# Optimization experiments

Measured on AMD Instinct MI355X. Metric: run time of the kernel, lower is better.

## Reference

```python
import jax, jax.numpy as jnp
import numpy as np
from itertools import product

L0 = (41, 1600, 1408)  # sparse_shape (z,y,x) from pc_range / voxel_size + [1,0,0]
B = 4
N_PER = 25000
PNAMES = ['w_in','s_in','b_in','w1','s1','b1','w2a','s2a','b2a','w2b','s2b','b2b','w2c','s2c','b2c','w3a','s3a','b3a','w3b','s3b','b3b','w3c','s3c','b3c','w4a','s4a','b4a','w4b','s4b','b4b','w4c','s4c','b4c','w_out','s_out','b_out']


def _enc(c, shape):
    D, H, W = shape
    return ((c[:, 0].astype(np.int64) * D + c[:, 1]) * H + c[:, 2]) * W + c[:, 3]


def _subm_rb(coords, shape):
    # submanifold conv rulebook: out site i gathers input j with coord_j = coord_i + offset
    N = coords.shape[0]
    keys = _enc(coords, shape)
    order = np.argsort(keys); sk = keys[order]
    ins, outs = [], []
    for dz, dy, dx in product((-1, 0, 1), repeat=3):
        nb = coords.astype(np.int64).copy()
        nb[:, 1] += dz; nb[:, 2] += dy; nb[:, 3] += dx
        ok = ((nb[:, 1] >= 0) & (nb[:, 1] < shape[0]) & (nb[:, 2] >= 0) & (nb[:, 2] < shape[1]) & (nb[:, 3] >= 0) & (nb[:, 3] < shape[2]))
        qi = np.nonzero(ok)[0]
        qk = _enc(nb[qi], shape)
        pos = np.clip(np.searchsorted(sk, qk), 0, N - 1)
        f = sk[pos] == qk
        ins.append(order[pos[f]].astype(np.int32))
        outs.append(qi[f].astype(np.int32))
    R = max(len(a) for a in ins)
    rin = np.zeros((27, R), np.int32); rout = np.full((27, R), N, np.int32)  # pad -> dummy out row
    for k in range(27):
        rin[k, :len(ins[k])] = ins[k]; rout[k, :len(outs[k])] = outs[k]
    return jnp.asarray(rin), jnp.asarray(rout)


def _spconv_rb(coords, shape, ks, st, pd):
    # strided sparse conv: out = (in + pad - k) / stride where divisible and in-bounds
    osh = tuple((shape[i] + 2 * pd[i] - ks[i]) // st[i] + 1 for i in range(3))
    per = []; allk = []
    for off in product(*[range(k) for k in ks]):
        oc = np.empty((coords.shape[0], 4), np.int64)
        oc[:, 0] = coords[:, 0]
        ok = np.ones(coords.shape[0], bool)
        for d in range(3):
            v = coords[:, d + 1].astype(np.int64) + pd[d] - off[d]
            ok &= (v % st[d] == 0)
            v = v // st[d]
            ok &= (v >= 0) & (v < osh[d])
            oc[:, d + 1] = v
        qi = np.nonzero(ok)[0]
        qk = _enc(oc[qi], osh)
        per.append((qi.astype(np.int32), qk)); allk.append(qk)
    uk = np.unique(np.concatenate(allk))
    Nout = len(uk); K = len(per)
    R = max(len(qi) for qi, _ in per)
    rin = np.zeros((K, R), np.int32); rout = np.full((K, R), Nout, np.int32)
    for k, (qi, qk) in enumerate(per):
        rin[k, :len(qi)] = qi
        rout[k, :len(qi)] = np.searchsorted(uk, qk).astype(np.int32)
    t = uk.copy()
    x = t % osh[2]; t //= osh[2]; y = t % osh[1]; t //= osh[1]; z = t % osh[0]; b = t // osh[0]
    ocoords = np.stack([b, z, y, x], 1).astype(np.int32)
    return jnp.asarray(rin), jnp.asarray(rout), ocoords, osh


def _gen_coords(rng):
    # clustered LiDAR-like voxel occupancy: gaussian clusters so 3x3x3 neighborhoods are populated
    out = []
    for b in range(B):
        nc = 250
        ctr = np.stack([rng.integers(6, 34, nc), rng.integers(60, 1540, nc), rng.integers(60, 1348, nc)], 1)
        pts = ctr[np.repeat(np.arange(nc), 400)] + rng.normal(0.0, 2.0, (nc * 400, 3))
        pts = np.rint(pts).astype(np.int64)
        for d in range(3):
            pts[:, d] = np.clip(pts[:, d], 0, L0[d] - 1)
        keys = (pts[:, 0] * L0[1] + pts[:, 1]) * L0[2] + pts[:, 2]
        _, ui = np.unique(keys, return_index=True)
        assert len(ui) >= N_PER
        c = pts[np.sort(ui[:N_PER])]
        out.append(np.concatenate([np.full((N_PER, 1), b, np.int64), c], 1))
    return np.concatenate(out, 0).astype(np.int32)


def _conv(feat, W, rin, rout, nout):
    # gather -> per-offset GEMM -> scatter-add (spconv rulebook algorithm)
    out = jnp.zeros((nout + 1, W.shape[2]), feat.dtype)  # +1 dummy row for padding
    for k in range(W.shape[0]):
        out = out.at[rout[k]].add(feat[rin[k]] @ W[k])
    return out[:nout]


def _bnrelu(x, s, b):
    # eval-mode BatchNorm1d folded to affine, then ReLU
    return jax.nn.relu(x * s + b)


def _net(voxels, normalizer, rb1_in, rb1_out, rb2s_in, rb2s_out, batch2, rb2_in, rb2_out, rb3s_in, rb3s_out, batch3, rb3_in, rb3_out, rb4s_in, rb4s_out, batch4, rb4_in, rb4_out, rbo_in, rbo_out, batch_out, P):
    n0 = voxels.shape[0]; n2 = batch2.shape[0]; n3 = batch3.shape[0]; n4 = batch4.shape[0]; no = batch_out.shape[0]
    f = voxels.sum(1) / normalizer  # mean VFE: (N0, 4)
    x = _bnrelu(_conv(f, P['w_in'], rb1_in, rb1_out, n0), P['s_in'], P['b_in'])
    x = _bnrelu(_conv(x, P['w1'], rb1_in, rb1_out, n0), P['s1'], P['b1'])
    x = _bnrelu(_conv(x, P['w2a'], rb2s_in, rb2s_out, n2), P['s2a'], P['b2a'])
    x = _bnrelu(_conv(x, P['w2b'], rb2_in, rb2_out, n2), P['s2b'], P['b2b'])
    x = _bnrelu(_conv(x, P['w2c'], rb2_in, rb2_out, n2), P['s2c'], P['b2c'])
    x = _bnrelu(_conv(x, P['w3a'], rb3s_in, rb3s_out, n3), P['s3a'], P['b3a'])
    x = _bnrelu(_conv(x, P['w3b'], rb3_in, rb3_out, n3), P['s3b'], P['b3b'])
    x = _bnrelu(_conv(x, P['w3c'], rb3_in, rb3_out, n3), P['s3c'], P['b3c'])
    x = _bnrelu(_conv(x, P['w4a'], rb4s_in, rb4s_out, n4), P['s4a'], P['b4a'])
    x = _bnrelu(_conv(x, P['w4b'], rb4_in, rb4_out, n4), P['s4b'], P['b4b'])
    x = _bnrelu(_conv(x, P['w4c'], rb4_in, rb4_out, n4), P['s4c'], P['b4c'])
    x = _bnrelu(_conv(x, P['w_out'], rbo_in, rbo_out, no), P['s_out'], P['b_out'])
    # per-batch global max pool over active voxels (== F.max_pool1d over voxel dim)
    return jax.ops.segment_max(x, batch_out.astype(jnp.int32), num_segments=B)


def setup_inputs():
    rng = np.random.default_rng(0)
    coords0 = _gen_coords(rng)
    rb1_in, rb1_out = _subm_rb(coords0, L0)
    rb2s_in, rb2s_out, c2, sh2 = _spconv_rb(coords0, L0, (3, 3, 3), (2, 2, 2), (1, 1, 1))
    rb2_in, rb2_out = _subm_rb(c2, sh2)
    rb3s_in, rb3s_out, c3, sh3 = _spconv_rb(c2, sh2, (3, 3, 3), (2, 2, 2), (1, 1, 1))
    rb3_in, rb3_out = _subm_rb(c3, sh3)
    rb4s_in, rb4s_out, c4, sh4 = _spconv_rb(c3, sh3, (3, 3, 3), (2, 2, 2), (0, 1, 1))
    rb4_in, rb4_out = _subm_rb(c4, sh4)
    rbo_in, rbo_out, co, _ = _spconv_rb(c4, sh4, (3, 1, 1), (2, 1, 1), (0, 0, 0))
    N0 = coords0.shape[0]
    d = dict(
        voxels=jnp.asarray(rng.normal(0, 1, (N0, 5, 4)).astype(np.float32)),
        voxel_num_points=jnp.asarray(rng.integers(1, 6, N0).astype(np.int32)),
        voxel_coords=jnp.asarray(coords0),
        rb1_in=rb1_in, rb1_out=rb1_out,
        rb2s_in=rb2s_in, rb2s_out=rb2s_out, batch2=jnp.asarray(c2[:, 0]),
        rb2_in=rb2_in, rb2_out=rb2_out,
        rb3s_in=rb3s_in, rb3s_out=rb3s_out, batch3=jnp.asarray(c3[:, 0]),
        rb3_in=rb3_in, rb3_out=rb3_out,
        rb4s_in=rb4s_in, rb4s_out=rb4s_out, batch4=jnp.asarray(c4[:, 0]),
        rb4_in=rb4_in, rb4_out=rb4_out,
        rbo_in=rbo_in, rbo_out=rbo_out, batch_out=jnp.asarray(co[:, 0]),
    )
    def _w(k, ci, co_):
        return jnp.asarray((rng.normal(0, 1, (k, ci, co_)) / np.sqrt(k * ci)).astype(np.float32))
    def _bn(c):
        return (jnp.asarray(rng.uniform(0.5, 1.5, c).astype(np.float32)), jnp.asarray(rng.normal(0, 0.1, c).astype(np.float32)))
    d['w_in'] = _w(27, 4, 16); d['s_in'], d['b_in'] = _bn(16)
    d['w1'] = _w(27, 16, 16); d['s1'], d['b1'] = _bn(16)
    d['w2a'] = _w(27, 16, 32); d['s2a'], d['b2a'] = _bn(32)
    d['w2b'] = _w(27, 32, 32); d['s2b'], d['b2b'] = _bn(32)
    d['w2c'] = _w(27, 32, 32); d['s2c'], d['b2c'] = _bn(32)
    d['w3a'] = _w(27, 32, 64); d['s3a'], d['b3a'] = _bn(64)
    d['w3b'] = _w(27, 64, 64); d['s3b'], d['b3b'] = _bn(64)
    d['w3c'] = _w(27, 64, 64); d['s3c'], d['b3c'] = _bn(64)
    d['w4a'] = _w(27, 64, 64); d['s4a'], d['b4a'] = _bn(64)
    d['w4b'] = _w(27, 64, 64); d['s4b'], d['b4b'] = _bn(64)
    d['w4c'] = _w(27, 64, 64); d['s4c'], d['b4c'] = _bn(64)
    d['w_out'] = _w(3, 64, 128); d['s_out'], d['b_out'] = _bn(128)
    return d


def reference(voxels, voxel_num_points, voxel_coords, rb1_in, rb1_out, rb2s_in, rb2s_out, batch2, rb2_in, rb2_out, rb3s_in, rb3s_out, batch3, rb3_in, rb3_out, rb4s_in, rb4s_out, batch4, rb4_in, rb4_out, rbo_in, rbo_out, batch_out, w_in, s_in, b_in, w1, s1, b1, w2a, s2a, b2a, w2b, s2b, b2b, w2c, s2c, b2c, w3a, s3a, b3a, w3b, s3b, b3b, w3c, s3c, b3c, w4a, s4a, b4a, w4b, s4b, b4b, w4c, s4c, b4c, w_out, s_out, b_out):
    normalizer = jnp.maximum(voxel_num_points.astype(voxels.dtype), 1.0)[:, None]
    P = dict(zip(PNAMES, (w_in, s_in, b_in, w1, s1, b1, w2a, s2a, b2a, w2b, s2b, b2b, w2c, s2c, b2c, w3a, s3a, b3a, w3b, s3b, b3b, w3c, s3c, b3c, w4a, s4a, b4a, w4b, s4b, b4b, w4c, s4c, b4c, w_out, s_out, b_out)))
    return _net(voxels, normalizer, rb1_in, rb1_out, rb2s_in, rb2s_out, batch2, rb2_in, rb2_out, rb3s_in, rb3s_out, batch3, rb3_in, rb3_out, rb4s_in, rb4s_out, batch4, rb4_in, rb4_out, rbo_in, rbo_out, batch_out, P)
```

## Files before the change

kernel.cpp:

```cpp
#include <hip/hip_runtime.h>
#include <cstddef>
#include <cstdint>

typedef _Float16 half8 __attribute__((ext_vector_type(8)));
typedef float floatx4 __attribute__((ext_vector_type(4)));
typedef float floatx16 __attribute__((ext_vector_type(16)));

static inline int cdiv_i(int a, int b) { return (a + b - 1) / b; }

struct RB { const int* rin; const int* rout; int K, R, nout, start, end, off; };
struct RBs { RB d[8]; };
__global__ void rb_fill_all(RBs P, int* __restrict__ tbl, int total) {
  int idx = blockIdx.x * blockDim.x + threadIdx.x;
  if (idx >= total) return;
#pragma unroll
  for (int l = 0; l < 8; ++l) {
    if (idx >= P.d[l].start && idx < P.d[l].end) {
      const RB rb = P.d[l];
      int e = idx - rb.start;
      int o = rb.rout[e];
      if ((unsigned)o < (unsigned)rb.nout) {
        int k = e / rb.R;
        tbl[rb.off + (size_t)k * rb.nout + o] = rb.rin[e];
      }
    }
  }
}

__global__ void tbl_fill_kernel(const int* __restrict__ rin,
                                const int* __restrict__ rout,
                                int* __restrict__ tbl, int K, int R, int nout) {
  int e = blockIdx.x * blockDim.x + threadIdx.x;
  if (e >= K * R) return;
  int o = rout[e];
  if ((unsigned)o >= (unsigned)nout) return;
  int k = e / R;
  tbl[(size_t)k * nout + o] = rin[e];
}

struct WP { const float* W; int K, Ci, CiPad, Co, start, end, off, p32; };
struct WPs {
  WP d[12];
  const float* vox; const int* vnp; _Float16* f0; int featTot, N0;
  float* dout; int outTot;
  int* tbl; int tblTot;
};
__global__ void prep_all(WPs P, _Float16* __restrict__ Bp, int total) {
  int idx = blockIdx.x * blockDim.x + threadIdx.x;
  if (idx >= total) return;
  if (idx < P.featTot) {
    int i = idx >> 3, c = idx & 7;
    float v = 0.f;
    if (i < P.N0 && c < 4) {
      const float* p = P.vox + (size_t)i * 20 + c;
      v = (p[0] + p[4] + p[8] + p[12] + p[16]) / fmaxf((float)P.vnp[i], 1.f);
    }
    P.f0[idx] = (_Float16)v;
    return;
  }
  idx -= P.featTot;
  if (idx < P.outTot) {
    P.dout[idx] = 0.f;
    return;
  }
  idx -= P.outTot;
  if (idx < P.tblTot) {
    P.tbl[idx] = -1;
    return;
  }
  int widx = idx - P.tblTot;
#pragma unroll
  for (int l = 0; l < 12; ++l) {
    if (widx >= P.d[l].start && widx < P.d[l].end) {
      const WP w = P.d[l];
      int e = widx - w.start;
      int j = e & 7;
      int lane = (e >> 3) & 63;
      int rest = e >> 9;
      float v;
      if (w.p32) {
        int NT = w.Co >> 5;
        int t = rest % NT, ch = rest / NT;
        int SUB = w.CiPad >> 4;
        int ko = ch / SUB, s = ch % SUB;
        int ci = s * 16 + ((lane >> 5) << 3) + j;
        int col = t * 32 + (lane & 31);
        v = w.W[((size_t)ko * w.Ci + ci) * w.Co + col];
      } else {
        int NT = w.Co >> 4;
        int t = rest % NT, ch = rest / NT;
        int kk = ch * 32 + ((lane >> 4) << 3) + j;
        int k = kk / w.CiPad, ci = kk % w.CiPad;
        int n = t * 16 + (lane & 15);
        v = (k < w.K && ci < w.Ci) ? w.W[((size_t)k * w.Ci + ci) * w.Co + n] : 0.f;
      }
      Bp[w.off + e] = (_Float16)v;
    }
  }
}

template <int K, int CiPad, int Co, int KS, int CG, int CBLK>
__global__ __launch_bounds__(256) void conv_mfma(
    const _Float16* __restrict__ feat, const _Float16* __restrict__ Bp,
    const int* __restrict__ tbl, const float* __restrict__ sc,
    const float* __restrict__ bi, _Float16* __restrict__ out,
    int nout, int nin) {
  constexpr int NT = Co / 16;
  constexpr int NTE = NT / CBLK;
  constexpr int NTW = NTE / CG;
  constexpr int RG = 4 / (KS * CG);
  static_assert(KS * CG * RG == 4 && RG >= 1 && NT % CBLK == 0 && NTE % CG == 0);
  constexpr int NCH = (K * CiPad + 31) / 32;
  constexpr int L2C = (CiPad == 8) ? 3 : 4;
  constexpr int DIV = (CiPad >= 32) ? (CiPad / 32) : 1;
  constexpr int CoP = NTE * 16 + 4;

  __shared__ float red[(KS > 1) ? (KS - 1) * RG * 16 * CoP : 1];

  if (blockIdx.x == 0 && threadIdx.x < Co)
    out[(size_t)nout * Co + threadIdx.x] = (_Float16)0.f;

  int id = blockIdx.x;
  { int nb = gridDim.x, nb8 = (nb >> 3) << 3;
    if (id < nb8) { int per = nb >> 3; id = (id & 7) * per + (id >> 3); } }
  const int rt = id / CBLK, cb = id % CBLK;
  const int wave = threadIdx.x >> 6, lane = threadIdx.x & 63;
  const int ks = wave % KS;
  const int cg = (wave / KS) % CG;
  const int rowg = wave / (KS * CG);
  const int m = lane & 15, lb = (lane >> 4) * 8;
  const int i0 = (rt * RG + rowg) * 16;
  if constexpr (KS == 1) { if (i0 >= nout) return; }
  const int row = i0 + m;
  const bool rOK = row < nout;
  const int ct0 = cb * NTE + cg * NTW;

  floatx4 acc[NTW];
#pragma unroll
  for (int n = 0; n < NTW; ++n) { floatx4 z = {0,0,0,0}; acc[n] = z; }

  if constexpr (CiPad >= 32) {
    constexpr int NKW = (K + KS - 1) / KS;
    constexpr int NC = NKW * DIV;
    constexpr int DA = NC < 8 ? NC : 8;
    constexpr int DB = NC < 2 ? NC : 2;
    int idx[NKW];
#pragma unroll
    for (int q = 0; q < NKW; ++q) {
      int k = ks * NKW + q;
      int jj = (rOK && k < K) ? tbl[(size_t)k * nout + row] : -1;
      idx[q] = (jj < 0) ? nin : jj;
    }
    half8 ap[DA]; half8 bq[DB][NTW];
#pragma unroll
    for (int d = 0; d < DA; ++d)
      ap[d] = *(const half8*)(feat + (size_t)idx[d / DIV] * CiPad + (d % DIV) * 32 + lb);
#pragma unroll
    for (int d = 0; d < DB; ++d) {
      int k = ks * NKW + d / DIV;
      int ch = ((k < K) ? k : (K - 1)) * DIV + (d % DIV);
#pragma unroll
      for (int n = 0; n < NTW; ++n)
        bq[d][n] = *(const half8*)(Bp + ((size_t)ch * NT * 64 + lane) * 8 +
                                   (size_t)(ct0 + n) * 512);
    }
#pragma unroll
    for (int ii = 0; ii < NC; ++ii) {
      half8 a = ap[ii % DA];
      half8 bt[NTW];
#pragma unroll
      for (int n = 0; n < NTW; ++n) bt[n] = bq[ii % DB][n];
      if (ii + DA < NC) {
        int nx = ii + DA;
        ap[ii % DA] = *(const half8*)(feat + (size_t)idx[nx / DIV] * CiPad +
                                      (nx % DIV) * 32 + lb);
      }
      if (ii + DB < NC) {
        int nx = ii + DB;
        int k = ks * NKW + nx / DIV;
        int ch = ((k < K) ? k : (K - 1)) * DIV + (nx % DIV);
#pragma unroll
        for (int n = 0; n < NTW; ++n)
          bq[ii % DB][n] = *(const half8*)(Bp + ((size_t)ch * NT * 64 + lane) * 8 +
                                           (size_t)(ct0 + n) * 512);
      }
#pragma unroll
      for (int n = 0; n < NTW; ++n)
        acc[n] = __builtin_amdgcn_mfma_f32_16x16x32_f16(a, bt[n], acc[n], 0, 0, 0);
    }
  } else {
    constexpr int NCW = (NCH + KS - 1) / KS;
    constexpr int DA = NCW < 8 ? NCW : 8;
    constexpr int DB = NCW < 2 ? NCW : 2;
    int idx[NCW];
#pragma unroll
    for (int q = 0; q < NCW; ++q) {
      int ch = ks * NCW + q;
      int ko = (ch * 32 + lb) >> L2C;
      int jj = (rOK && ko < K && ch < NCH) ? tbl[(size_t)ko * nout + row] : -1;
      idx[q] = (jj < 0) ? nin : jj;
    }
    half8 ap[DA]; half8 bq[DB][NTW];
#pragma unroll
    for (int d = 0; d < DA; ++d) {
      int ch = ks * NCW + d;
      ap[d] = *(const half8*)(feat + (size_t)idx[d] * CiPad + ((ch * 32 + lb) & (CiPad - 1)));
    }
#pragma unroll
    for (int d = 0; d < DB; ++d) {
      int ch = ks * NCW + d;
      if (ch >= NCH) ch = NCH - 1;
#pragma unroll
      for (int n = 0; n < NTW; ++n)
        bq[d][n] = *(const half8*)(Bp + ((size_t)ch * NT * 64 + lane) * 8 +
                                   (size_t)(ct0 + n) * 512);
    }
#pragma unroll
    for (int ii = 0; ii < NCW; ++ii) {
      half8 a = ap[ii % DA];
      half8 bt[NTW];
#pragma unroll
      for (int n = 0; n < NTW; ++n) bt[n] = bq[ii % DB][n];
      if (ii + DA < NCW) {
        int nx = ii + DA;
        int ch = ks * NCW + nx;
        ap[ii % DA] = *(const half8*)(feat + (size_t)idx[nx] * CiPad +
                                      ((ch * 32 + lb) & (CiPad - 1)));
      }
      if (ii + DB < NCW) {
        int nx = ii + DB;
        int ch = ks * NCW + nx;
        if (ch >= NCH) ch = NCH - 1;
#pragma unroll
        for (int n = 0; n < NTW; ++n)
          bq[ii % DB][n] = *(const half8*)(Bp + ((size_t)ch * NT * 64 + lane) * 8 +
                                           (size_t)(ct0 + n) * 512);
      }
#pragma unroll
      for (int n = 0; n < NTW; ++n)
        acc[n] = __builtin_amdgcn_mfma_f32_16x16x32_f16(a, bt[n], acc[n], 0, 0, 0);
    }
  }

  const int rl = (lane >> 4) * 4;
  if constexpr (KS > 1) {
    if (ks > 0) {
#pragma unroll
      for (int n = 0; n < NTW; ++n) {
        int lcol = (cg * NTW + n) * 16 + m;
#pragma unroll
        for (int r = 0; r < 4; ++r)
          red[((ks - 1) * RG + rowg) * 16 * CoP + (rl + r) * CoP + lcol] = acc[n][r];
      }
    }
    __syncthreads();
    if (ks > 0) return;
#pragma unroll
    for (int s = 1; s < KS; ++s)
#pragma unroll
      for (int n = 0; n < NTW; ++n) {
        int lcol = (cg * NTW + n) * 16 + m;
#pragma unroll
        for (int r = 0; r < 4; ++r)
          acc[n][r] += red[((s - 1) * RG + rowg) * 16 * CoP + (rl + r) * CoP + lcol];
      }
  }

#pragma unroll
  for (int n = 0; n < NTW; ++n) {
    int col = (ct0 + n) * 16 + m;
    float s_ = sc[col], b_ = bi[col];
#pragma unroll
    for (int r = 0; r < 4; ++r) {
      int orow = i0 + rl + r;
      if (orow < nout)
        out[(size_t)orow * Co + col] = (_Float16)fmaxf(fmaf(acc[n][r], s_, b_), 0.f);
    }
  }
}

template <int K, int CiPad, int Co, int KS, int CG, int CBLK>
__global__ __launch_bounds__(256) void conv_mfma32(
    const _Float16* __restrict__ feat, const _Float16* __restrict__ Bp,
    const int* __restrict__ tbl, const float* __restrict__ sc,
    const float* __restrict__ bi, _Float16* __restrict__ out,
    int nout, int nin) {
  constexpr int NT = Co / 32;
  constexpr int NTE = NT / CBLK;
  constexpr int NTW = NTE / CG;
  constexpr int RG = 4 / (KS * CG);
  static_assert(KS * CG * RG == 4 && RG >= 1 && NT % CBLK == 0 && NTE % CG == 0 && NTW >= 1);
  constexpr int SUB = CiPad / 16;
  constexpr int NKW = (K + KS - 1) / KS;
  constexpr int NC = NKW * SUB;
  constexpr int DA = NC < 8 ? NC : 8;
  constexpr int DB = NC < 2 ? NC : 2;
  constexpr int CoP = NTE * 32 + 4;

  __shared__ float red[(KS > 1) ? (KS - 1) * RG * 32 * CoP : 1];

  if (blockIdx.x == 0 && threadIdx.x < Co)
    out[(size_t)nout * Co + threadIdx.x] = (_Float16)0.f;

  int id = blockIdx.x;
  { int nb = gridDim.x, nb8 = (nb >> 3) << 3;
    if (id < nb8) { int per = nb >> 3; id = (id & 7) * per + (id >> 3); } }
  const int rt = id / CBLK, cb = id % CBLK;
  const int wave = threadIdx.x >> 6, lane = threadIdx.x & 63;
  const int ks = wave % KS;
  const int cg = (wave / KS) % CG;
  const int rowg = wave / (KS * CG);
  const int m = lane & 31, lb = (lane >> 5) * 8, h = lane >> 5;
  const int i0 = (rt * RG + rowg) * 32;
  if constexpr (KS == 1) { if (i0 >= nout) return; }
  const int row = i0 + m;
  const bool rOK = row < nout;
  const int ct0 = cb * NTE + cg * NTW;

  floatx16 acc[NTW];
#pragma unroll
  for (int n = 0; n < NTW; ++n)
#pragma unroll
    for (int r = 0; r < 16; ++r) acc[n][r] = 0.f;

  int idx[NKW];
#pragma unroll
  for (int q = 0; q < NKW; ++q) {
    int k = ks * NKW + q;
    int jj = (rOK && k < K) ? tbl[(size_t)k * nout + row] : -1;
    idx[q] = (jj < 0) ? nin : jj;
  }

  half8 ap[DA]; half8 bq[DB][NTW];
#pragma unroll
  for (int d = 0; d < DA; ++d)
    ap[d] = *(const half8*)(feat + (size_t)idx[d / SUB] * CiPad + (d % SUB) * 16 + lb);
#pragma unroll
  for (int d = 0; d < DB; ++d) {
    int k = ks * NKW + d / SUB;
    int ch = ((k < K) ? k : (K - 1)) * SUB + (d % SUB);
#pragma unroll
    for (int n = 0; n < NTW; ++n)
      bq[d][n] = *(const half8*)(Bp + (size_t)(ch * NT + ct0 + n) * 512 + lane * 8);
  }
#pragma unroll
  for (int ii = 0; ii < NC; ++ii) {
    half8 a = ap[ii % DA];
    half8 bt[NTW];
#pragma unroll
    for (int n = 0; n < NTW; ++n) bt[n] = bq[ii % DB][n];
    if (ii + DA < NC) {
      int nx = ii + DA;
      ap[ii % DA] = *(const half8*)(feat + (size_t)idx[nx / SUB] * CiPad +
                                    (nx % SUB) * 16 + lb);
    }
    if (ii + DB < NC) {
      int nx = ii + DB;
      int k = ks * NKW + nx / SUB;
      int ch = ((k < K) ? k : (K - 1)) * SUB + (nx % SUB);
#pragma unroll
      for (int n = 0; n < NTW; ++n)
        bq[ii % DB][n] = *(const half8*)(Bp + (size_t)(ch * NT + ct0 + n) * 512 + lane * 8);
    }
#pragma unroll
    for (int n = 0; n < NTW; ++n)
      acc[n] = __builtin_amdgcn_mfma_f32_32x32x16_f16(a, bt[n], acc[n], 0, 0, 0);
  }

  if constexpr (KS > 1) {
    if (ks > 0) {
#pragma unroll
      for (int n = 0; n < NTW; ++n) {
        int lcol = (cg * NTW + n) * 32 + m;
#pragma unroll
        for (int reg = 0; reg < 16; ++reg) {
          int r = (reg & 3) + 8 * (reg >> 2) + 4 * h;
          red[((ks - 1) * RG + rowg) * 32 * CoP + r * CoP + lcol] = acc[n][reg];
        }
      }
    }
    __syncthreads();
    if (ks > 0) return;
#pragma unroll
    for (int s = 1; s < KS; ++s)
#pragma unroll
      for (int n = 0; n < NTW; ++n) {
        int lcol = (cg * NTW + n) * 32 + m;
#pragma unroll
        for (int reg = 0; reg < 16; ++reg) {
          int r = (reg & 3) + 8 * (reg >> 2) + 4 * h;
          acc[n][reg] += red[((s - 1) * RG + rowg) * 32 * CoP + r * CoP + lcol];
        }
      }
  }

#pragma unroll
  for (int n = 0; n < NTW; ++n) {
    int col = (ct0 + n) * 32 + m;
    float s_ = sc[col], b_ = bi[col];
#pragma unroll
    for (int reg = 0; reg < 16; ++reg) {
      int orow = i0 + (reg & 3) + 8 * (reg >> 2) + 4 * h;
      if (orow < nout)
        out[(size_t)orow * Co + col] = (_Float16)fmaxf(fmaf(acc[n][reg], s_, b_), 0.f);
    }
  }
}

__global__ __launch_bounds__(256) void segmax2(const _Float16* __restrict__ x,
                                               const int* __restrict__ batch,
                                               int n, float* __restrict__ out) {
  const int RPB = 128;
  int c = threadIdx.x & 127, g = threadIdx.x >> 7;
  int r0 = blockIdx.x * RPB + g;
  int rend = min(n, blockIdx.x * RPB + RPB);
  float mx = 0.f;
  int cb = -1;
  for (int r = r0; r < rend; r += 2) {
    int b = batch[r];
    if (b != cb) {
      if (cb >= 0) atomicMax((int*)out + ((size_t)cb << 7) + c, __float_as_int(mx));
      cb = b; mx = 0.f;
    }
    mx = fmaxf(mx, (float)x[(size_t)r * 128 + c]);
  }
  if (cb >= 0) atomicMax((int*)out + ((size_t)cb << 7) + c, __float_as_int(mx));
}

extern "C" void kernel_launch(void* const* d_in, const int* in_sizes, int n_in,
                              void* d_out, int out_size, void* d_ws, size_t ws_size,
                              hipStream_t stream) {
  auto I = [&](int idx) { return (const int*)d_in[idx]; };
  auto F = [&](int idx) { return (const float*)d_in[idx]; };

  const int N0  = in_sizes[1];
  const int R1  = in_sizes[3] / 27;
  const int R2s = in_sizes[5] / 27;
  const int n2  = in_sizes[7];
  const int R2  = in_sizes[8] / 27;
  const int R3s = in_sizes[10] / 27;
  const int n3  = in_sizes[12];
  const int R3  = in_sizes[13] / 27;
  const int R4s = in_sizes[15] / 27;
  const int n4  = in_sizes[17];
  const int R4  = in_sizes[18] / 27;
  const int Ro  = in_sizes[20] / 3;
  const int no  = in_sizes[22];

  const int wIdx[12] = {23, 26, 29, 32, 35, 38, 41, 44, 47, 50, 53, 56};
  const int Ks[12]   = {27, 27, 27, 27, 27, 27, 27, 27, 27, 27, 27, 3};
  const int Cis[12]  = {4, 16, 16, 32, 32, 32, 64, 64, 64, 64, 64, 64};
  const int Cos[12]  = {16, 16, 32, 32, 32, 64, 64, 64, 64, 64, 64, 128};
  const int P32[12]  = {0, 0, 0, 1, 1, 1, 1, 1, 1, 1, 1, 0};
  WPs P;
  int wtot = 0;
  int bpOff[12];
  for (int l = 0; l < 12; ++l) {
    int cip = Cis[l] < 8 ? 8 : Cis[l];
    int sz;
    if (P32[l]) sz = Ks[l] * (cip / 16) * (Cos[l] / 32) * 512;
    else        sz = ((Ks[l] * cip + 31) / 32) * (Cos[l] / 16) * 512;
    P.d[l].W = F(wIdx[l]);
    P.d[l].K = Ks[l]; P.d[l].Ci = Cis[l]; P.d[l].CiPad = cip; P.d[l].Co = Cos[l];
    P.d[l].start = wtot; P.d[l].end = wtot + sz; P.d[l].off = wtot; P.d[l].p32 = P32[l];
    bpOff[l] = wtot;
    wtot += sz;
  }

  RBs RP;
  const int rbRin[8]  = {3, 5, 8, 10, 13, 15, 18, 20};
  const int rbRs[8]   = {R1, R2s, R2, R3s, R3, R4s, R4, Ro};
  const int rbKs[8]   = {27, 27, 27, 27, 27, 27, 27, 3};
  const int rbNout[8] = {N0, n2, n2, n3, n3, n4, n4, no};
  size_t tblInts[8], tblOff[8];
  size_t totTbl = 0;
  int totFill = 0;
  for (int l = 0; l < 8; ++l) {
    tblInts[l] = (size_t)rbNout[l] * rbKs[l];
    tblOff[l] = totTbl;
    totTbl += tblInts[l];
    RP.d[l].rin = I(rbRin[l]);
    RP.d[l].rout = I(rbRin[l] + 1);
    RP.d[l].K = rbKs[l]; RP.d[l].R = rbRs[l]; RP.d[l].nout = rbNout[l];
    RP.d[l].start = totFill;
    totFill += rbKs[l] * rbRs[l];
    RP.d[l].end = totFill;
    RP.d[l].off = (int)tblOff[l];
  }

  size_t S = (size_t)(N0 + 1) * 16;
  auto smax = [&](size_t v) { if (v > S) S = v; };
  smax((size_t)(n2 + 1) * 32);
  smax((size_t)(n3 + 1) * 64);
  smax((size_t)(n4 + 1) * 64);
  smax((size_t)(no + 1) * 128);
  S = (S + 7) & ~(size_t)7;

  _Float16* h = (_Float16*)d_ws;
  size_t off = 0;
  _Float16* f0 = h + off;   off += (size_t)(N0 + 1) * 8;
  _Float16* bufA = h + off; off += S;
  _Float16* bufB = h + off; off += S;
  _Float16* Bp = h + off;   off += (size_t)((wtot + 7) & ~7);
  int* tblBase = (int*)(h + off);
  size_t usedBytes = off * 2;
  bool prebuilt = (usedBytes + totTbl * 4 <= ws_size);

  P.vox = F(0); P.vnp = I(1); P.f0 = f0;
  P.featTot = (N0 + 1) * 8; P.N0 = N0;
  P.dout = (float*)d_out; P.outTot = out_size;
  if (prebuilt) { P.tbl = tblBase; P.tblTot = (int)totTbl; }
  else          { P.tbl = nullptr; P.tblTot = 0; }
  int prepTot = P.featTot + P.outTot + P.tblTot + wtot;
  prep_all<<<cdiv_i(prepTot, 256), 256, 0, stream>>>(P, Bp, prepTot);

  const int l2rb[12] = {0, 0, 1, 2, 2, 3, 4, 4, 5, 6, 6, 7};
  const int* tblL[12];
  if (prebuilt) {
    rb_fill_all<<<cdiv_i(totFill, 256), 256, 0, stream>>>(RP, tblBase, totFill);
    for (int l = 0; l < 12; ++l) tblL[l] = tblBase + tblOff[l2rb[l]];
  } else {
    for (int l = 0; l < 12; ++l) tblL[l] = tblBase;
  }
  auto buildSeq = [&](int rb) {
    if (prebuilt) return;
    hipMemsetAsync(tblBase, 0xFF, tblInts[rb] * 4, stream);
    tbl_fill_kernel<<<cdiv_i(rbKs[rb] * rbRs[rb], 256), 256, 0, stream>>>(
        I(rbRin[rb]), I(rbRin[rb] + 1), tblBase, rbKs[rb], rbRs[rb], rbNout[rb]);
  };

#define CONV16(Kk, CIP, CO, KSv, CGv, CBv, IN, LI, OUTB, NOUT, NIN)           \
  do {                                                                        \
    constexpr int rowsPerBlk = (4 / (KSv * CGv)) * 16;                        \
    int nblk = cdiv_i(NOUT, rowsPerBlk) * CBv;                                \
    conv_mfma<Kk, CIP, CO, KSv, CGv, CBv><<<nblk, 256, 0, stream>>>(          \
        IN, Bp + bpOff[LI], tblL[LI], F(wIdx[LI] + 1), F(wIdx[LI] + 2),       \
        OUTB, NOUT, NIN);                                                     \
  } while (0)
#define CONV32(Kk, CIP, CO, KSv, CGv, CBv, IN, LI, OUTB, NOUT, NIN)           \
  do {                                                                        \
    constexpr int rowsPerBlk = (4 / (KSv * CGv)) * 32;                        \
    int nblk = cdiv_i(NOUT, rowsPerBlk) * CBv;                                \
    conv_mfma32<Kk, CIP, CO, KSv, CGv, CBv><<<nblk, 256, 0, stream>>>(        \
        IN, Bp + bpOff[LI], tblL[LI], F(wIdx[LI] + 1), F(wIdx[LI] + 2),       \
        OUTB, NOUT, NIN);                                                     \
  } while (0)

  buildSeq(0);
  CONV16(27, 8, 16, 1, 1, 1, f0, 0, bufA, N0, N0);
  CONV16(27, 16, 16, 2, 1, 1, bufA, 1, bufB, N0, N0);
  buildSeq(1);
  CONV16(27, 16, 32, 2, 1, 1, bufB, 2, bufA, n2, N0);
  buildSeq(2);
  CONV32(27, 32, 32, 4, 1, 1, bufA, 3, bufB, n2, n2);
  CONV32(27, 32, 32, 4, 1, 1, bufB, 4, bufA, n2, n2);
  buildSeq(3);
  CONV32(27, 32, 64, 4, 1, 2, bufA, 5, bufB, n3, n2);
  buildSeq(4);
  CONV32(27, 64, 64, 4, 1, 2, bufB, 6, bufA, n3, n3);
  CONV32(27, 64, 64, 4, 1, 2, bufA, 7, bufB, n3, n3);
  buildSeq(5);
  CONV32(27, 64, 64, 4, 1, 2, bufB, 8, bufA, n4, n3);
  buildSeq(6);
  CONV32(27, 64, 64, 4, 1, 2, bufA, 9, bufB, n4, n4);
  CONV32(27, 64, 64, 4, 1, 2, bufB, 10, bufA, n4, n4);
  buildSeq(7);
  CONV16(3, 64, 128, 2, 2, 2, bufA, 11, bufB, no, n4);
  segmax2<<<cdiv_i(no, 128), 256, 0, stream>>>(bufB, I(22), no, (float*)d_out);
#undef CONV16
#undef CONV32
}
```

Baseline: 442.3 us.

## Fuse tail sparse conv layers and segmax into one persistent kernel with grid barriers

Replaces the last seven conv launches and the segment-max launch with a single persistent kernel of 256 blocks. Inside it, each wave loops over output tiles and the layers are separated by atomic grid-wide barriers. The barrier counters are zeroed in the prep kernel. This targets launch overhead and tail idle time on the small downsampled layers. The trade-offs are that it gives up the earlier per-layer block tuning (split-K, LDS reductions), and it relies on all 256 blocks being co-resident; if they are not, the barriers deadlock. It also removes the fallback path for when the rulebook tables do not fit in the workspace.

Result: slower. 620.9 us (+40.4%).

```diff
diff --git a/kernel.cpp b/kernel.cpp
--- a/kernel.cpp
+++ b/kernel.cpp
@@ -27,23 +27,13 @@
   }
 }
 
-__global__ void tbl_fill_kernel(const int* __restrict__ rin,
-                                const int* __restrict__ rout,
-                                int* __restrict__ tbl, int K, int R, int nout) {
-  int e = blockIdx.x * blockDim.x + threadIdx.x;
-  if (e >= K * R) return;
-  int o = rout[e];
-  if ((unsigned)o >= (unsigned)nout) return;
-  int k = e / R;
-  tbl[(size_t)k * nout + o] = rin[e];
-}
-
 struct WP { const float* W; int K, Ci, CiPad, Co, start, end, off, p32; };
 struct WPs {
   WP d[12];
   const float* vox; const int* vnp; _Float16* f0; int featTot, N0;
   float* dout; int outTot;
   int* tbl; int tblTot;
+  int* bar;
 };
 __global__ void prep_all(WPs P, _Float16* __restrict__ Bp, int total) {
   int idx = blockIdx.x * blockDim.x + threadIdx.x;
@@ -59,16 +49,12 @@
     return;
   }
   idx -= P.featTot;
-  if (idx < P.outTot) {
-    P.dout[idx] = 0.f;
-    return;
-  }
+  if (idx < P.outTot) { P.dout[idx] = 0.f; return; }
   idx -= P.outTot;
-  if (idx < P.tblTot) {
-    P.tbl[idx] = -1;
-    return;
-  }
-  int widx = idx - P.tblTot;
+  if (idx < P.tblTot) { P.tbl[idx] = -1; return; }
+  idx -= P.tblTot;
+  if (idx < 16) { P.bar[idx] = 0; return; }
+  int widx = idx - 16;
 #pragma unroll
   for (int l = 0; l < 12; ++l) {
     if (widx >= P.d[l].start && widx < P.d[l].end) {
@@ -407,24 +393,221 @@
   }
 }
 
-__global__ __launch_bounds__(256) void segmax2(const _Float16* __restrict__ x,
-                                               const int* __restrict__ batch,
-                                               int n, float* __restrict__ out) {
-  const int RPB = 128;
-  int c = threadIdx.x & 127, g = threadIdx.x >> 7;
-  int r0 = blockIdx.x * RPB + g;
-  int rend = min(n, blockIdx.x * RPB + RPB);
-  float mx = 0.f;
-  int cb = -1;
-  for (int r = r0; r < rend; r += 2) {
-    int b = batch[r];
-    if (b != cb) {
-      if (cb >= 0) atomicMax((int*)out + ((size_t)cb << 7) + c, __float_as_int(mx));
-      cb = b; mx = 0.f;
-    }
-    mx = fmaxf(mx, (float)x[(size_t)r * 128 + c]);
-  }
-  if (cb >= 0) atomicMax((int*)out + ((size_t)cb << 7) + c, __float_as_int(mx));
+
+struct LCfg {
+  const _Float16* fin; _Float16* fout; const _Float16* bp;
+  const int* tbl; const float* sc; const float* bi; int nout, nin;
+};
+struct TK {
+  LCfg L[7];
+  const int* batch; int no; float* dout;
+  int* bar; int nblk;
+};
+
+__device__ __forceinline__ void gsync(int* c, int nblk) {
+  __syncthreads();
+  if (threadIdx.x == 0) {
+    __builtin_amdgcn_fence(__ATOMIC_RELEASE, "agent");
+    __hip_atomic_fetch_add(c, 1, __ATOMIC_RELAXED, __HIP_MEMORY_SCOPE_AGENT);
+    while (__hip_atomic_load(c, __ATOMIC_RELAXED, __HIP_MEMORY_SCOPE_AGENT) < nblk)
+      __builtin_amdgcn_s_sleep(8);
+    __builtin_amdgcn_fence(__ATOMIC_ACQUIRE, "agent");
+  }
+  __syncthreads();
+}
+
+template <int K, int CiPad, int Co, int CB>
+__device__ void conv16_layer(const LCfg L, int gw, int GW) {
+  constexpr int NT = Co / 16;
+  constexpr int NTW = NT / CB;
+  static_assert(NT % CB == 0 && NTW >= 1);
+  constexpr int DIV = CiPad / 32;
+  const int lane = threadIdx.x & 63;
+  const int m = lane & 15, lb = (lane >> 4) * 8;
+  if (gw == 0) {
+    for (int c = lane; c < Co; c += 64)
+      L.fout[(size_t)L.nout * Co + c] = (_Float16)0.f;
+  }
+  const int ntile = ((L.nout + 15) >> 4) * CB;
+  for (int it = gw; it < ntile; it += GW) {
+    const int rt = it / CB, cb = it % CB;
+    const int i0 = rt * 16;
+    const int row = i0 + m;
+    const bool rOK = row < L.nout;
+    const int ct0 = cb * NTW;
+    floatx4 acc[NTW];
+#pragma unroll
+    for (int n = 0; n < NTW; ++n) { floatx4 z = {0, 0, 0, 0}; acc[n] = z; }
+
+    constexpr int NC = K * DIV;
+    constexpr int DA = NC < 8 ? NC : 8;
+    constexpr int DB = NC < 2 ? NC : 2;
+    int idx[K];
+#pragma unroll
+    for (int q = 0; q < K; ++q) {
+      int jj = rOK ? L.tbl[(size_t)q * L.nout + row] : -1;
+      idx[q] = (jj < 0) ? L.nin : jj;
+    }
+    half8 ap[DA]; half8 bq[DB][NTW];
+#pragma unroll
+    for (int d = 0; d < DA; ++d)
+      ap[d] = *(const half8*)(L.fin + (size_t)idx[d / DIV] * CiPad + (d % DIV) * 32 + lb);
+#pragma unroll
+    for (int d = 0; d < DB; ++d) {
+#pragma unroll
+      for (int n = 0; n < NTW; ++n)
+        bq[d][n] = *(const half8*)(L.bp + ((size_t)d * NT * 64 + lane) * 8 +
+                                   (size_t)(ct0 + n) * 512);
+    }
+#pragma unroll
+    for (int ii = 0; ii < NC; ++ii) {
+      half8 a = ap[ii % DA];
+      half8 bt[NTW];
+#pragma unroll
+      for (int n = 0; n < NTW; ++n) bt[n] = bq[ii % DB][n];
+      if (ii + DA < NC) {
+        int nx = ii + DA;
+        ap[ii % DA] = *(const half8*)(L.fin + (size_t)idx[nx / DIV] * CiPad +
+                                      (nx % DIV) * 32 + lb);
+      }
+      if (ii + DB < NC) {
+        int nx = ii + DB;
+#pragma unroll
+        for (int n = 0; n < NTW; ++n)
+          bq[ii % DB][n] = *(const half8*)(L.bp + ((size_t)nx * NT * 64 + lane) * 8 +
+                                           (size_t)(ct0 + n) * 512);
+      }
+#pragma unroll
+      for (int n = 0; n < NTW; ++n)
+        acc[n] = __builtin_amdgcn_mfma_f32_16x16x32_f16(a, bt[n], acc[n], 0, 0, 0);
+    }
+
+    const int rl = (lane >> 4) * 4;
+#pragma unroll
+    for (int n = 0; n < NTW; ++n) {
+      int col = (ct0 + n) * 16 + m;
+      float s_ = L.sc[col], b_ = L.bi[col];
+#pragma unroll
+      for (int r = 0; r < 4; ++r) {
+        int orow = i0 + rl + r;
+        if (orow < L.nout)
+          L.fout[(size_t)orow * Co + col] = (_Float16)fmaxf(fmaf(acc[n][r], s_, b_), 0.f);
+      }
+    }
+  }
+}
+
+template <int K, int CiPad, int Co, int CB>
+__device__ void conv32_layer(const LCfg L, int gw, int GW) {
+  constexpr int NT = Co / 32;
+  constexpr int NTW = NT / CB;
+  static_assert(NT % CB == 0 && NTW >= 1);
+  constexpr int SUB = CiPad / 16;
+  constexpr int NC = K * SUB;
+  constexpr int DA = NC < 8 ? NC : 8;
+  constexpr int DB = NC < 2 ? NC : 2;
+  const int lane = threadIdx.x & 63;
+  const int m = lane & 31, lb = (lane >> 5) * 8, h = lane >> 5;
+  if (gw == 0) {
+    for (int c = lane; c < Co; c += 64)
+      L.fout[(size_t)L.nout * Co + c] = (_Float16)0.f;
+  }
+  const int ntile = ((L.nout + 31) >> 5) * CB;
+  for (int it = gw; it < ntile; it += GW) {
+    const int rt = it / CB, cb = it % CB;
+    const int i0 = rt * 32;
+    const int row = i0 + m;
+    const bool rOK = row < L.nout;
+    const int ct0 = cb * NTW;
+    floatx16 acc[NTW];
+#pragma unroll
+    for (int n = 0; n < NTW; ++n)
+#pragma unroll
+      for (int r = 0; r < 16; ++r) acc[n][r] = 0.f;
+
+    int idx[K];
+#pragma unroll
+    for (int q = 0; q < K; ++q) {
+      int jj = rOK ? L.tbl[(size_t)q * L.nout + row] : -1;
+      idx[q] = (jj < 0) ? L.nin : jj;
+    }
+    half8 ap[DA]; half8 bq[DB][NTW];
+#pragma unroll
+    for (int d = 0; d < DA; ++d)
+      ap[d] = *(const half8*)(L.fin + (size_t)idx[d / SUB] * CiPad + (d % SUB) * 16 + lb);
+#pragma unroll
+    for (int d = 0; d < DB; ++d) {
+#pragma unroll
+      for (int n = 0; n < NTW; ++n)
+        bq[d][n] = *(const half8*)(L.bp + (size_t)(d * NT + ct0 + n) * 512 + lane * 8);
+    }
+#pragma unroll
+    for (int ii = 0; ii < NC; ++ii) {
+      half8 a = ap[ii % DA];
+      half8 bt[NTW];
+#pragma unroll
+      for (int n = 0; n < NTW; ++n) bt[n] = bq[ii % DB][n];
+      if (ii + DA < NC) {
+        int nx = ii + DA;
+        ap[ii % DA] = *(const half8*)(L.fin + (size_t)idx[nx / SUB] * CiPad +
+                                      (nx % SUB) * 16 + lb);
+      }
+      if (ii + DB < NC) {
+        int nx = ii + DB;
+#pragma unroll
+        for (int n = 0; n < NTW; ++n)
+          bq[ii % DB][n] = *(const half8*)(L.bp + (size_t)(nx * NT + ct0 + n) * 512 + lane * 8);
+      }
+#pragma unroll
+      for (int n = 0; n < NTW; ++n)
+        acc[n] = __builtin_amdgcn_mfma_f32_32x32x16_f16(a, bt[n], acc[n], 0, 0, 0);
+    }
+
+#pragma unroll
+    for (int n = 0; n < NTW; ++n) {
+      int col = (ct0 + n) * 32 + m;
+      float s_ = L.sc[col], b_ = L.bi[col];
+#pragma unroll
+      for (int reg = 0; reg < 16; ++reg) {
+        int orow = i0 + (reg & 3) + 8 * (reg >> 2) + 4 * h;
+        if (orow < L.nout)
+          L.fout[(size_t)orow * Co + col] = (_Float16)fmaxf(fmaf(acc[n][reg], s_, b_), 0.f);
+      }
+    }
+  }
+}
+
+__global__ __launch_bounds__(512, 2) void tail_persistent(TK P) {
+  const int nblk = P.nblk;
+  const int gw = blockIdx.x * 8 + (threadIdx.x >> 6);
+  const int GW = gridDim.x * 8;
+  conv32_layer<27, 32, 64, 2>(P.L[0], gw, GW); gsync(P.bar + 0, nblk);
+  conv32_layer<27, 64, 64, 2>(P.L[1], gw, GW); gsync(P.bar + 1, nblk);
+  conv32_layer<27, 64, 64, 2>(P.L[2], gw, GW); gsync(P.bar + 2, nblk);
+  conv32_layer<27, 64, 64, 2>(P.L[3], gw, GW); gsync(P.bar + 3, nblk);
+  conv32_layer<27, 64, 64, 2>(P.L[4], gw, GW); gsync(P.bar + 4, nblk);
+  conv32_layer<27, 64, 64, 2>(P.L[5], gw, GW); gsync(P.bar + 5, nblk);
+  conv16_layer<3, 64, 128, 4>(P.L[6], gw, GW); gsync(P.bar + 6, nblk);
+  {
+    const _Float16* x = (const _Float16*)P.L[6].fout;
+    int c = threadIdx.x & 127;
+    int g = blockIdx.x * 4 + (threadIdx.x >> 7);
+    int G = gridDim.x * 4;
+    int per = (P.no + G - 1) / G;
+    int r0 = g * per;
+    int rend = min(P.no, r0 + per);
+    float mx = 0.f;
+    int cb = -1;
+    for (int r = r0; r < rend; ++r) {
+      int b = P.batch[r];
+      if (b != cb) {
+        if (cb >= 0) atomicMax((int*)P.dout + ((size_t)cb << 7) + c, __float_as_int(mx));
+        cb = b; mx = 0.f;
+      }
+      mx = fmaxf(mx, (float)x[(size_t)r * 128 + c]);
+    }
+    if (cb >= 0) atomicMax((int*)P.dout + ((size_t)cb << 7) + c, __float_as_int(mx));
+  }
 }
 
 extern "C" void kernel_launch(void* const* d_in, const int* in_sizes, int n_in,
@@ -472,13 +655,12 @@
   const int rbRs[8]   = {R1, R2s, R2, R3s, R3, R4s, R4, Ro};
   const int rbKs[8]   = {27, 27, 27, 27, 27, 27, 27, 3};
   const int rbNout[8] = {N0, n2, n2, n3, n3, n4, n4, no};
-  size_t tblInts[8], tblOff[8];
+  size_t tblOff[8];
   size_t totTbl = 0;
   int totFill = 0;
   for (int l = 0; l < 8; ++l) {
-    tblInts[l] = (size_t)rbNout[l] * rbKs[l];
     tblOff[l] = totTbl;
-    totTbl += tblInts[l];
+    totTbl += (size_t)rbNout[l] * rbKs[l];
     RP.d[l].rin = I(rbRin[l]);
     RP.d[l].rout = I(rbRin[l] + 1);
     RP.d[l].K = rbKs[l]; RP.d[l].R = rbRs[l]; RP.d[l].nout = rbNout[l];
@@ -503,31 +685,21 @@
   _Float16* bufB = h + off; off += S;
   _Float16* Bp = h + off;   off += (size_t)((wtot + 7) & ~7);
   int* tblBase = (int*)(h + off);
-  size_t usedBytes = off * 2;
-  bool prebuilt = (usedBytes + totTbl * 4 <= ws_size);
+  int* bar = tblBase + totTbl;
 
   P.vox = F(0); P.vnp = I(1); P.f0 = f0;
   P.featTot = (N0 + 1) * 8; P.N0 = N0;
   P.dout = (float*)d_out; P.outTot = out_size;
-  if (prebuilt) { P.tbl = tblBase; P.tblTot = (int)totTbl; }
-  else          { P.tbl = nullptr; P.tblTot = 0; }
-  int prepTot = P.featTot + P.outTot + P.tblTot + wtot;
+  P.tbl = tblBase; P.tblTot = (int)totTbl;
+  P.bar = bar;
+  int prepTot = P.featTot + P.outTot + P.tblTot + 16 + wtot;
   prep_all<<<cdiv_i(prepTot, 256), 256, 0, stream>>>(P, Bp, prepTot);
+
+  rb_fill_all<<<cdiv_i(totFill, 256), 256, 0, stream>>>(RP, tblBase, totFill);
 
   const int l2rb[12] = {0, 0, 1, 2, 2, 3, 4, 4, 5, 6, 6, 7};
   const int* tblL[12];
-  if (prebuilt) {
-    rb_fill_all<<<cdiv_i(totFill, 256), 256, 0, stream>>>(RP, tblBase, totFill);
-    for (int l = 0; l < 12; ++l) tblL[l] = tblBase + tblOff[l2rb[l]];
-  } else {
-    for (int l = 0; l < 12; ++l) tblL[l] = tblBase;
-  }
-  auto buildSeq = [&](int rb) {
-    if (prebuilt) return;
-    hipMemsetAsync(tblBase, 0xFF, tblInts[rb] * 4, stream);
-    tbl_fill_kernel<<<cdiv_i(rbKs[rb] * rbRs[rb], 256), 256, 0, stream>>>(
-        I(rbRin[rb]), I(rbRin[rb] + 1), tblBase, rbKs[rb], rbRs[rb], rbNout[rb]);
-  };
+  for (int l = 0; l < 12; ++l) tblL[l] = tblBase + tblOff[l2rb[l]];
 
 #define CONV16(Kk, CIP, CO, KSv, CGv, CBv, IN, LI, OUTB, NOUT, NIN)           \
   do {                                                                        \
@@ -546,27 +718,33 @@
         OUTB, NOUT, NIN);                                                     \
   } while (0)
 
-  buildSeq(0);
   CONV16(27, 8, 16, 1, 1, 1, f0, 0, bufA, N0, N0);
   CONV16(27, 16, 16, 2, 1, 1, bufA, 1, bufB, N0, N0);
-  buildSeq(1);
   CONV16(27, 16, 32, 2, 1, 1, bufB, 2, bufA, n2, N0);
-  buildSeq(2);
   CONV32(27, 32, 32, 4, 1, 1, bufA, 3, bufB, n2, n2);
   CONV32(27, 32, 32, 4, 1, 1, bufB, 4, bufA, n2, n2);
-  buildSeq(3);
-  CONV32(27, 32, 64, 4, 1, 2, bufA, 5, bufB, n3, n2);
-  buildSeq(4);
-  CONV32(27, 64, 64, 4, 1, 2, bufB, 6, bufA, n3, n3);
-  CONV32(27, 64, 64, 4, 1, 2, bufA, 7, bufB, n3, n3);
-  buildSeq(5);
-  CONV32(27, 64, 64, 4, 1, 2, bufB, 8, bufA, n4, n3);
-  buildSeq(6);
-  CONV32(27, 64, 64, 4, 1, 2, bufA, 9, bufB, n4, n4);
-  CONV32(27, 64, 64, 4, 1, 2, bufB, 10, bufA, n4, n4);
-  buildSeq(7);
-  CONV16(3, 64, 128, 2, 2, 2, bufA, 11, bufB, no, n4);
-  segmax2<<<cdiv_i(no, 128), 256, 0, stream>>>(bufB, I(22), no, (float*)d_out);
 #undef CONV16
 #undef CONV32
-}
+
+  TK T;
+  const int tl[7]     = {5, 6, 7, 8, 9, 10, 11};
+  const int touts[7]  = {n3, n3, n3, n4, n4, n4, no};
+  const int tins[7]   = {n2, n3, n3, n3, n4, n4, n4};
+  _Float16* tb[8];
+  tb[0] = bufA;
+  for (int i = 0; i < 7; ++i) tb[i + 1] = (i & 1) ? bufA : bufB;
+  for (int i = 0; i < 7; ++i) {
+    int l = tl[i];
+    T.L[i].fin  = tb[i];
+    T.L[i].fout = tb[i + 1];
+    T.L[i].bp   = Bp + bpOff[l];
+    T.L[i].tbl  = tblL[l];
+    T.L[i].sc   = F(wIdx[l] + 1);
+    T.L[i].bi   = F(wIdx[l] + 2);
+    T.L[i].nout = touts[i];
+    T.L[i].nin  = tins[i];
+  }
+  T.batch = I(22); T.no = no; T.dout = (float*)d_out;
+  T.bar = bar; T.nblk = 256;
+  tail_persistent<<<256, 512, 0, stream>>>(T);
+}
```
